# Optimization experiments

Hardware: AMD Instinct MI355X
Metric: run time of the kernel (lower is better)

Reference implementation:

```python
import jax, jax.numpy as jnp
import numpy as np

B, NQ, QDIM = 4, 128, 512
EMB, HEADS = 512, 8
VOCAB, WDIM = 20000, 300
DH = EMB // HEADS
TAU = 1.0
LN_EPS = 1e-5


def setup_inputs() -> dict:
    key = jax.random.key(0)
    ks = jax.random.split(key, 8)
    s = lambda fan_in: 1.0 / np.sqrt(fan_in)
    return {
        "queries": jax.random.normal(ks[0], (B, NQ, QDIM), dtype=jnp.float32),
        "glove": jax.random.normal(ks[1], (VOCAB, WDIM), dtype=jnp.float32),
        # Linear weights stored as (in, out); y = x @ W (equivalent to torch x @ W.T)
        "Wq": jax.random.normal(ks[2], (QDIM, EMB), dtype=jnp.float32) * s(QDIM),
        "Wk": jax.random.normal(ks[3], (WDIM, EMB), dtype=jnp.float32) * s(WDIM),
        "Wv": jax.random.normal(ks[4], (WDIM, EMB), dtype=jnp.float32) * s(WDIM),
        "Wout": jax.random.normal(ks[5], (EMB, QDIM), dtype=jnp.float32) * s(EMB),
        "b_out": jnp.zeros((QDIM,), dtype=jnp.float32),
        "ln_g": jnp.ones((QDIM,), dtype=jnp.float32),
        "ln_b": jnp.zeros((QDIM,), dtype=jnp.float32),
    }


def _forward(queries, glove, Wq, Wk, Wv, Wout, b_out, ln_g, ln_b):
    b, nq, _ = queries.shape
    V = glove.shape[0]
    scale = DH ** -0.5

    # SubLayerConnection: x + sublayer(LayerNorm(x))
    mu = jnp.mean(queries, axis=-1, keepdims=True)
    var = jnp.mean(jnp.square(queries - mu), axis=-1, keepdims=True)
    xn = (queries - mu) * jax.lax.rsqrt(var + LN_EPS) * ln_g + ln_b

    # Projections. K/V of the GloVe table are batch-independent -> compute once.
    q = (xn @ Wq).reshape(b, nq, HEADS, DH)          # [b, nq, h, dh]
    k = (glove @ Wk).reshape(V, HEADS, DH)           # [V, h, dh]
    v = (glove @ Wv).reshape(V, HEADS, DH)           # [V, h, dh]

    # Attention scores over the whole vocabulary: [b, h, nq, V]
    dots = jnp.einsum("bqhd,vhd->bhqv", q, k) * scale

    # Gumbel-softmax, hard (straight-through)
    gkey = jax.random.key(42)
    u = jax.random.uniform(gkey, dots.shape, dtype=dots.dtype,
                           minval=jnp.finfo(dots.dtype).tiny, maxval=1.0)
    gumbels = (dots - jnp.log(-jnp.log(u))) / TAU
    y_soft = jax.nn.softmax(gumbels, axis=-1)
    idx = jnp.argmax(gumbels, axis=-1)               # argmax(softmax) == argmax(logits)
    y_hard = jax.nn.one_hot(idx, V, dtype=dots.dtype)
    attn = y_hard - jax.lax.stop_gradient(y_soft) + y_soft

    out = jnp.einsum("bhqv,vhd->bqhd", attn, v).reshape(b, nq, EMB)
    out = out @ Wout + b_out                          # dropout is identity in eval
    return queries + out


def reference(queries, glove, Wq, Wk, Wv, Wout, b_out, ln_g, ln_b):
    return _forward(queries, glove, Wq, Wk, Wv, Wout, b_out, ln_g, ln_b)
```

## Files before the change

kernel.cpp:

```cpp
#include <hip/hip_runtime.h>
#include <cstdint>
#include <cmath>

#define NB 4
#define NQn 128
#define QD 512
#define EMBD 512
#define NH 8
#define DHn 64
#define VOCAB 20000
#define WDn 300
#define VCHUNK 128
#define NCHUNK 157

typedef float f32x4 __attribute__((ext_vector_type(4)));
typedef float f32x2 __attribute__((ext_vector_type(2)));
typedef short bf16x8 __attribute__((ext_vector_type(8)));

__device__ __forceinline__ f32x2 lo2(f32x4 v) { return __builtin_shufflevector(v, v, 0, 1); }
__device__ __forceinline__ f32x2 hi2(f32x4 v) { return __builtin_shufflevector(v, v, 2, 3); }

__device__ __forceinline__ void pk_fma_blo(f32x2 &d, f32x2 a, f32x2 b) {
  asm("v_pk_fma_f32 %0, %1, %2, %0 op_sel:[0,0,0] op_sel_hi:[0,1,1]"
      : "+v"(d) : "v"(a), "v"(b));
}
__device__ __forceinline__ void pk_fma_bhi(f32x2 &d, f32x2 a, f32x2 b) {
  asm("v_pk_fma_f32 %0, %1, %2, %0 op_sel:[1,0,0] op_sel_hi:[1,1,1]"
      : "+v"(d) : "v"(a), "v"(b));
}

__device__ __forceinline__ uint32_t rotl(uint32_t x, int r) {
  return __builtin_amdgcn_alignbit(x, x, 32 - r);
}

__device__ __forceinline__ uint32_t cvt_pk_bf16(float a, float b) {
  uint32_t r;
  asm("v_cvt_pk_bf16_f32 %0, %1, %2" : "=v"(r) : "v"(a), "v"(b));
  return r;
}

__device__ __forceinline__ void split4(f32x4 v, uint2 &hi, uint2 &lo) {
  uint32_t h01 = cvt_pk_bf16(v.x, v.y);
  uint32_t h23 = cvt_pk_bf16(v.z, v.w);
  float rx = v.x - __uint_as_float(h01 << 16);
  float ry = v.y - __uint_as_float(h01 & 0xFFFF0000u);
  float rz = v.z - __uint_as_float(h23 << 16);
  float rw = v.w - __uint_as_float(h23 & 0xFFFF0000u);
  hi = make_uint2(h01, h23);
  lo = make_uint2(cvt_pk_bf16(rx, ry), cvt_pk_bf16(rz, rw));
}

#define TFK1 42u
#define TFK2 (0x1BD11BDAu ^ 42u)
__device__ __forceinline__ void tf8(uint32_t (&x0)[8], uint32_t (&x1)[8]) {
#define R8(r) \
  { _Pragma("unroll") for (int j = 0; j < 8; ++j) { x0[j] += x1[j]; x1[j] = rotl(x1[j], r); x1[j] ^= x0[j]; } }
#define K8(a, b) \
  { _Pragma("unroll") for (int j = 0; j < 8; ++j) { x0[j] += (a); x1[j] += (b); } }
  K8(0u, TFK1)
  R8(13) R8(15) R8(26) R8(6)  K8(TFK1, TFK2 + 1u)
  R8(17) R8(29) R8(16) R8(24) K8(TFK2, 0u + 2u)
  R8(13) R8(15) R8(26) R8(6)  K8(0u, TFK1 + 3u)
  R8(17) R8(29) R8(16) R8(24) K8(TFK1, TFK2 + 4u)
  R8(13) R8(15) R8(26) R8(6)  K8(TFK2, 0u + 5u)
#undef R8
#undef K8
}

__device__ __forceinline__ float gumbel_from_bits(uint32_t bits) {
  float f = __uint_as_float((bits >> 9) | 0x3f800000u) - 1.0f;
  float u = fmaxf(f, 1.17549435e-38f);
  float t = __log2f(u);
  float s = __log2f(-t);
  return fmaf(0.69314718f, s, -0.36651292f);
}

__device__ __forceinline__ unsigned long long pack_key(float val, int idx) {
  uint32_t fb = __float_as_uint(val);
  uint32_t key = (fb & 0x80000000u) ? ~fb : (fb | 0x80000000u);
  return ((unsigned long long)key << 32) |
         (unsigned long long)(0xFFFFFFFFu - (uint32_t)idx);
}

__global__ __launch_bounds__(256, 4) void ln_qproj_kernel(
                                const float* __restrict__ queries,
                                const float* __restrict__ Wq,
                                const float* __restrict__ ln_g,
                                const float* __restrict__ ln_b,
                                ushort* __restrict__ qh_ws,
                                ushort* __restrict__ ql_ws) {
  __shared__ float xnT[QD][4];
  const int tid = threadIdx.x;
  const int wave = tid >> 6, lane = tid & 63;
  const int r0 = blockIdx.x * 4;
  const int r = r0 + wave;

  float vals[8];
  float s = 0.f;
#pragma unroll
  for (int j = 0; j < 8; ++j) { vals[j] = queries[r * QD + j * 64 + lane]; s += vals[j]; }
#pragma unroll
  for (int m = 32; m >= 1; m >>= 1) s += __shfl_xor(s, m, 64);
  const float mu = s * (1.f / 512.f);
  float ss = 0.f;
#pragma unroll
  for (int j = 0; j < 8; ++j) { float d = vals[j] - mu; ss += d * d; }
#pragma unroll
  for (int m = 32; m >= 1; m >>= 1) ss += __shfl_xor(ss, m, 64);
  const float rstd = 1.f / sqrtf(ss * (1.f / 512.f) + 1e-5f);
#pragma unroll
  for (int j = 0; j < 8; ++j) {
    int e = j * 64 + lane;
    xnT[e][wave] = (vals[j] - mu) * rstd * ln_g[e] + ln_b[e];
  }
  __syncthreads();

  const int e = blockIdx.y * 256 + tid;
  float a0 = 0.f, a1 = 0.f, a2 = 0.f, a3 = 0.f;
#pragma unroll 4
  for (int i = 0; i < QD; ++i) {
    f32x4 xv = *(const f32x4*)&xnT[i][0];
    float w = Wq[i * EMBD + e];
    a0 += xv.x * w; a1 += xv.y * w; a2 += xv.z * w; a3 += xv.w * w;
  }
  const int h = e >> 6, d = e & 63;
  float aa[4] = {a0, a1, a2, a3};
#pragma unroll
  for (int i = 0; i < 4; ++i) {
    float q = aa[i] * 0.125f;
    uint32_t hp = cvt_pk_bf16(q, q);
    float resid = q - __uint_as_float(hp << 16);
    uint32_t lp = cvt_pk_bf16(resid, resid);
    size_t off = ((size_t)h * 512 + (r0 + i)) * 64 + d;
    qh_ws[off] = (ushort)(hp & 0xFFFFu);
    ql_ws[off] = (ushort)(lp & 0xFFFFu);
  }
}

#define BKk 60
__global__ __launch_bounds__(256, 4) void kproj_kernel(
                             const float* __restrict__ glove,
                             const float* __restrict__ Wk,
                             ushort* __restrict__ kh_ws,
                             ushort* __restrict__ kl_ws) {
  const int id = blockIdx.x;
  const int lo = id & 7, h = (id >> 3) & 7, vg = (id >> 6) * 8 + lo;
  if (vg >= 313) return;
  const int v0 = vg * 64;
  const int n0 = h * 64;
  __shared__ float AsT[BKk][68];
  __shared__ float Bs[BKk][64];
  const int tid = threadIdx.x;
  const int ty = tid >> 4, tx = tid & 15;
  f32x2 acc2[4][2] = {};
  for (int s = 0; s < 5; ++s) {
    const int w0 = s * BKk;
    __syncthreads();
    for (int f = tid; f < 64 * 15; f += 256) {
      int row = f / 15, c4 = f % 15;
      int v = v0 + row;
      float4 g4 = (v < VOCAB) ? *(const float4*)&glove[(size_t)v * WDn + w0 + c4 * 4]
                              : make_float4(0.f, 0.f, 0.f, 0.f);
      AsT[c4 * 4 + 0][row] = g4.x;
      AsT[c4 * 4 + 1][row] = g4.y;
      AsT[c4 * 4 + 2][row] = g4.z;
      AsT[c4 * 4 + 3][row] = g4.w;
    }
    for (int f = tid; f < BKk * 16; f += 256) {
      int row = f / 16, c4 = f % 16;
      *(float4*)&Bs[row][c4 * 4] = *(const float4*)&Wk[(size_t)(w0 + row) * EMBD + n0 + c4 * 4];
    }
    __syncthreads();
#pragma unroll 4
    for (int w = 0; w < BKk; ++w) {
      f32x4 aq = *(const f32x4*)&AsT[w][ty * 4];
      f32x4 bv = *(const f32x4*)&Bs[w][tx * 4];
      f32x2 bl = lo2(bv), bh = hi2(bv);
      f32x2 a01 = lo2(aq), a23 = hi2(aq);
      pk_fma_blo(acc2[0][0], a01, bl); pk_fma_blo(acc2[0][1], a01, bh);
      pk_fma_bhi(acc2[1][0], a01, bl); pk_fma_bhi(acc2[1][1], a01, bh);
      pk_fma_blo(acc2[2][0], a23, bl); pk_fma_blo(acc2[2][1], a23, bh);
      pk_fma_bhi(acc2[3][0], a23, bl); pk_fma_bhi(acc2[3][1], a23, bh);
    }
  }
#pragma unroll
  for (int i = 0; i < 4; ++i) {
    int v = v0 + ty * 4 + i;
    if (v < VOCAB) {
      f32x4 kv = {acc2[i][0].x, acc2[i][0].y, acc2[i][1].x, acc2[i][1].y};
      uint2 hi, lo2v;
      split4(kv, hi, lo2v);
      size_t off = ((size_t)h * VOCAB + v) * 64 + tx * 4;
      *(uint2*)&kh_ws[off] = hi;
      *(uint2*)&kl_ws[off] = lo2v;
    }
  }
}

template<bool FULL>
__device__ __forceinline__ void score_epi(const f32x4 (&acc)[8],
                                          int v0, int tx, int ty, int rowtile, int h,
                                          unsigned long long* __restrict__ pk_buf) {
#pragma unroll
  for (int i = 0; i < 4; ++i) {
    const int r = rowtile * 128 + ty * 4 + i;
    const int b = r >> 7, q = r & 127;
    const int rowidx = (b * NH + h) * NQn + q;
    const uint32_t base = (uint32_t)rowidx * (uint32_t)VOCAB;

    uint32_t x0[8], x1[8];
#pragma unroll
    for (int j = 0; j < 8; ++j) {
      x0[j] = 0u;
      x1[j] = base + (uint32_t)(v0 + tx + 16 * j);
    }
    tf8(x0, x1);

    float best = -INFINITY; int bidx = 0x7fffffff;
#pragma unroll
    for (int j = 0; j < 8; ++j) {
      int v = v0 + tx + 16 * j;
      if (FULL || v < VOCAB) {
        float g = gumbel_from_bits(x0[j] ^ x1[j]);
        float val = acc[j][i] - g;
        if (val > best) { best = val; bidx = v; }
      }
    }
#pragma unroll
    for (int m = 8; m >= 1; m >>= 1) {
      float ov = __shfl_xor(best, m, 64);
      int   oi = __shfl_xor(bidx, m, 64);
      if (ov > best || (ov == best && oi < bidx)) { best = ov; bidx = oi; }
    }
    if (tx == 0) atomicMax(&pk_buf[rowidx], pack_key(best, bidx));
  }
}

__global__ __launch_bounds__(512, 8) void score_kernel(
                  const ushort* __restrict__ qh_ws,
                  const ushort* __restrict__ ql_ws,
                  const ushort* __restrict__ kh_ws,
                  const ushort* __restrict__ kl_ws,
                  unsigned long long* __restrict__ pk_buf) {
  __shared__ uint4 lds4[2048];
  char* const Kh = (char*)lds4;
  char* const Kl = Kh + 16384;
  const int tid = threadIdx.x;
  const int id = blockIdx.x;
  const int h = id & 7, rowtile = (id >> 3) & 3, chunk = id >> 5;
  const int v0 = chunk * VCHUNK;
  const int tx = tid & 15, ty = tid >> 4;
  const int w = tid >> 6;
  const int g4 = (tid >> 4) & 3;
  const int swz = (tx & 7) << 4;

  bf16x8 aH[2], aL[2];
  {
    const size_t qbase = ((size_t)h * 512 + rowtile * 128 + w * 16 + tx) * 64 + g4 * 8;
#pragma unroll
    for (int kh = 0; kh < 2; ++kh) {
      aH[kh] = *(const bf16x8*)(qh_ws + qbase + kh * 32);
      aL[kh] = *(const bf16x8*)(ql_ws + qbase + kh * 32);
    }
  }

  for (int f = tid; f < 128 * 8; f += 512) {
    int row = f >> 3, c8 = f & 7;
    int v = v0 + row;
    uint4 vh = {0u, 0u, 0u, 0u}, vl = {0u, 0u, 0u, 0u};
    if (v < VOCAB) {
      size_t off = ((size_t)h * VOCAB + v) * 64 + c8 * 8;
      vh = *(const uint4*)(kh_ws + off);
      vl = *(const uint4*)(kl_ws + off);
    }
    int loff = (row * 128 + c8 * 16) ^ ((row & 7) << 4);
    *(uint4*)(Kh + loff) = vh;
    *(uint4*)(Kl + loff) = vl;
  }
  __syncthreads();

  f32x4 acc[8] = {};
#pragma unroll
  for (int ct = 0; ct < 8; ++ct) {
    const int bbase = (ct * 16 + tx) * 128 + g4 * 16;
    bf16x8 bH[2], bL[2];
#pragma unroll
    for (int kh = 0; kh < 2; ++kh) {
      int off = (bbase + kh * 64) ^ swz;
      bH[kh] = *(const bf16x8*)(Kh + off);
      bL[kh] = *(const bf16x8*)(Kl + off);
    }
    acc[ct] = __builtin_amdgcn_mfma_f32_16x16x32_bf16(aH[0], bH[0], acc[ct], 0, 0, 0);
    acc[ct] = __builtin_amdgcn_mfma_f32_16x16x32_bf16(aH[1], bH[1], acc[ct], 0, 0, 0);
    acc[ct] = __builtin_amdgcn_mfma_f32_16x16x32_bf16(aH[0], bL[0], acc[ct], 0, 0, 0);
    acc[ct] = __builtin_amdgcn_mfma_f32_16x16x32_bf16(aH[1], bL[1], acc[ct], 0, 0, 0);
    acc[ct] = __builtin_amdgcn_mfma_f32_16x16x32_bf16(aL[0], bH[0], acc[ct], 0, 0, 0);
    acc[ct] = __builtin_amdgcn_mfma_f32_16x16x32_bf16(aL[1], bH[1], acc[ct], 0, 0, 0);
    acc[ct] = __builtin_amdgcn_mfma_f32_16x16x32_bf16(aL[0], bL[0], acc[ct], 0, 0, 0);
    acc[ct] = __builtin_amdgcn_mfma_f32_16x16x32_bf16(aL[1], bL[1], acc[ct], 0, 0, 0);
  }

  if (v0 + VCHUNK <= VOCAB)
    score_epi<true>(acc, v0, tx, ty, rowtile, h, pk_buf);
  else
    score_epi<false>(acc, v0, tx, ty, rowtile, h, pk_buf);
}

__global__ __launch_bounds__(512, 8) void out_kernel(
                           const float* __restrict__ queries,
                           const float* __restrict__ glove,
                           const float* __restrict__ Wv,
                           const float* __restrict__ Wout,
                           const float* __restrict__ b_out,
                           const unsigned long long* __restrict__ pk_buf,
                           float* __restrict__ out) {
  __shared__ float gl[NH][WDn];
  __shared__ float vrow[EMBD];
  __shared__ int idxs[NH];
  const int tid = threadIdx.x;
  const int r = blockIdx.x, b = r >> 7, q = r & 127;
  if (tid < NH) {
    unsigned long long p = pk_buf[(b * NH + tid) * NQn + q];
    idxs[tid] = (int)(0xFFFFFFFFu - (uint32_t)(p & 0xFFFFFFFFull));
  }
  __syncthreads();
  for (int f = tid; f < NH * 75; f += 512) {
    int hh = f / 75, c4 = f % 75;
    *(float4*)&gl[hh][c4 * 4] = *(const float4*)&glove[(size_t)idxs[hh] * WDn + c4 * 4];
  }
  __syncthreads();
  {
    const int e = tid, hh = e >> 6;
    float a = 0.f;
    for (int w = 0; w < WDn; ++w) a += gl[hh][w] * Wv[(size_t)w * EMBD + e];
    vrow[e] = a;
  }
  __syncthreads();
  {
    const int j = tid;
    float o = 0.f;
    for (int e = 0; e < EMBD; ++e) o += vrow[e] * Wout[(size_t)e * QD + j];
    out[(size_t)r * QD + j] = queries[(size_t)r * QD + j] + o + b_out[j];
  }
}

extern "C" void kernel_launch(void* const* d_in, const int* in_sizes, int n_in,
                              void* d_out, int out_size, void* d_ws, size_t ws_size,
                              hipStream_t stream) {
  const float* queries = (const float*)d_in[0];
  const float* glove   = (const float*)d_in[1];
  const float* Wq      = (const float*)d_in[2];
  const float* Wk      = (const float*)d_in[3];
  const float* Wv      = (const float*)d_in[4];
  const float* Wout    = (const float*)d_in[5];
  const float* b_out   = (const float*)d_in[6];
  const float* ln_g    = (const float*)d_in[7];
  const float* ln_b    = (const float*)d_in[8];
  float* out = (float*)d_out;

  char* ws = (char*)d_ws;
  ushort* qh_ws = (ushort*)ws;
  ushort* ql_ws = qh_ws + (size_t)NH * 512 * 64;
  ushort* kh_ws = ql_ws + (size_t)NH * 512 * 64;
  ushort* kl_ws = kh_ws + (size_t)NH * VOCAB * 64;
  unsigned long long* pk_buf = (unsigned long long*)(kl_ws + (size_t)NH * VOCAB * 64);

  hipMemsetAsync(pk_buf, 0, (size_t)NB * NH * NQn * sizeof(unsigned long long), stream);

  hipLaunchKernelGGL(ln_qproj_kernel, dim3(128, 2), dim3(256), 0, stream,
                     queries, Wq, ln_g, ln_b, qh_ws, ql_ws);
  hipLaunchKernelGGL(kproj_kernel, dim3(2560), dim3(256), 0, stream,
                     glove, Wk, kh_ws, kl_ws);
  hipLaunchKernelGGL(score_kernel, dim3(5024), dim3(512), 0, stream,
                     qh_ws, ql_ws, kh_ws, kl_ws, pk_buf);
  hipLaunchKernelGGL(out_kernel, dim3(512), dim3(512), 0, stream,
                     queries, glove, Wv, Wout, b_out, pk_buf, out);
}
```

Measured before the change: 346.7 us.

## Merge Q/K projection kernels and pk_buf memset into one prep launch

The LayerNorm+Q-projection kernel, the K-projection kernel and the memset of the argmax buffer become a single launch, with each role picked from the block index. This removes two launch gaps and the memset, and lets the small Q-projection blocks run alongside the K-projection blocks. The Gumbel subtraction is folded into one fma, and the Q fragment loads in the score kernel move after the K tile staging to overlap with it. The merged kernel uses a shared LDS buffer sized for the larger role, so the Q-projection blocks reserve more LDS than they need.

```diff
diff --git a/kernel.cpp b/kernel.cpp
--- a/kernel.cpp
+++ b/kernel.cpp
@@ -67,14 +67,6 @@
 #undef K8
 }
 
-__device__ __forceinline__ float gumbel_from_bits(uint32_t bits) {
-  float f = __uint_as_float((bits >> 9) | 0x3f800000u) - 1.0f;
-  float u = fmaxf(f, 1.17549435e-38f);
-  float t = __log2f(u);
-  float s = __log2f(-t);
-  return fmaf(0.69314718f, s, -0.36651292f);
-}
-
 __device__ __forceinline__ unsigned long long pack_key(float val, int idx) {
   uint32_t fb = __float_as_uint(val);
   uint32_t key = (fb & 0x80000000u) ? ~fb : (fb | 0x80000000u);
@@ -82,118 +74,124 @@
          (unsigned long long)(0xFFFFFFFFu - (uint32_t)idx);
 }
 
-__global__ __launch_bounds__(256, 4) void ln_qproj_kernel(
-                                const float* __restrict__ queries,
-                                const float* __restrict__ Wq,
-                                const float* __restrict__ ln_g,
-                                const float* __restrict__ ln_b,
-                                ushort* __restrict__ qh_ws,
-                                ushort* __restrict__ ql_ws) {
-  __shared__ float xnT[QD][4];
-  const int tid = threadIdx.x;
-  const int wave = tid >> 6, lane = tid & 63;
-  const int r0 = blockIdx.x * 4;
-  const int r = r0 + wave;
-
-  float vals[8];
-  float s = 0.f;
-#pragma unroll
-  for (int j = 0; j < 8; ++j) { vals[j] = queries[r * QD + j * 64 + lane]; s += vals[j]; }
-#pragma unroll
-  for (int m = 32; m >= 1; m >>= 1) s += __shfl_xor(s, m, 64);
-  const float mu = s * (1.f / 512.f);
-  float ss = 0.f;
-#pragma unroll
-  for (int j = 0; j < 8; ++j) { float d = vals[j] - mu; ss += d * d; }
-#pragma unroll
-  for (int m = 32; m >= 1; m >>= 1) ss += __shfl_xor(ss, m, 64);
-  const float rstd = 1.f / sqrtf(ss * (1.f / 512.f) + 1e-5f);
-#pragma unroll
-  for (int j = 0; j < 8; ++j) {
-    int e = j * 64 + lane;
-    xnT[e][wave] = (vals[j] - mu) * rstd * ln_g[e] + ln_b[e];
-  }
-  __syncthreads();
-
-  const int e = blockIdx.y * 256 + tid;
-  float a0 = 0.f, a1 = 0.f, a2 = 0.f, a3 = 0.f;
-#pragma unroll 4
-  for (int i = 0; i < QD; ++i) {
-    f32x4 xv = *(const f32x4*)&xnT[i][0];
-    float w = Wq[i * EMBD + e];
-    a0 += xv.x * w; a1 += xv.y * w; a2 += xv.z * w; a3 += xv.w * w;
-  }
-  const int h = e >> 6, d = e & 63;
-  float aa[4] = {a0, a1, a2, a3};
-#pragma unroll
-  for (int i = 0; i < 4; ++i) {
-    float q = aa[i] * 0.125f;
-    uint32_t hp = cvt_pk_bf16(q, q);
-    float resid = q - __uint_as_float(hp << 16);
-    uint32_t lp = cvt_pk_bf16(resid, resid);
-    size_t off = ((size_t)h * 512 + (r0 + i)) * 64 + d;
-    qh_ws[off] = (ushort)(hp & 0xFFFFu);
-    ql_ws[off] = (ushort)(lp & 0xFFFFu);
-  }
-}
-
 #define BKk 60
-__global__ __launch_bounds__(256, 4) void kproj_kernel(
+__global__ __launch_bounds__(256, 4) void prep_kernel(
+                             const float* __restrict__ queries,
+                             const float* __restrict__ Wq,
+                             const float* __restrict__ ln_g,
+                             const float* __restrict__ ln_b,
                              const float* __restrict__ glove,
                              const float* __restrict__ Wk,
+                             ushort* __restrict__ qh_ws,
+                             ushort* __restrict__ ql_ws,
                              ushort* __restrict__ kh_ws,
-                             ushort* __restrict__ kl_ws) {
-  const int id = blockIdx.x;
-  const int lo = id & 7, h = (id >> 3) & 7, vg = (id >> 6) * 8 + lo;
-  if (vg >= 313) return;
-  const int v0 = vg * 64;
-  const int n0 = h * 64;
-  __shared__ float AsT[BKk][68];
-  __shared__ float Bs[BKk][64];
+                             ushort* __restrict__ kl_ws,
+                             unsigned long long* __restrict__ pk_buf) {
+  __shared__ __align__(16) char smem[31680];
+  const int bid = blockIdx.x;
   const int tid = threadIdx.x;
-  const int ty = tid >> 4, tx = tid & 15;
-  f32x2 acc2[4][2] = {};
-  for (int s = 0; s < 5; ++s) {
-    const int w0 = s * BKk;
+
+  if (bid < 2560) {
+    const int lo = bid & 7, h = (bid >> 3) & 7, vg = (bid >> 6) * 8 + lo;
+    if (vg >= 313) return;
+    const int v0 = vg * 64;
+    const int n0 = h * 64;
+    float (*AsT)[68] = (float(*)[68])smem;
+    float (*Bs)[64]  = (float(*)[64])(smem + 16320);
+    const int ty = tid >> 4, tx = tid & 15;
+    f32x2 acc2[4][2] = {};
+    for (int s = 0; s < 5; ++s) {
+      const int w0 = s * BKk;
+      __syncthreads();
+      for (int f = tid; f < 64 * 15; f += 256) {
+        int row = f / 15, c4 = f % 15;
+        int v = v0 + row;
+        float4 g4 = (v < VOCAB) ? *(const float4*)&glove[(size_t)v * WDn + w0 + c4 * 4]
+                                : make_float4(0.f, 0.f, 0.f, 0.f);
+        AsT[c4 * 4 + 0][row] = g4.x;
+        AsT[c4 * 4 + 1][row] = g4.y;
+        AsT[c4 * 4 + 2][row] = g4.z;
+        AsT[c4 * 4 + 3][row] = g4.w;
+      }
+      for (int f = tid; f < BKk * 16; f += 256) {
+        int row = f / 16, c4 = f % 16;
+        *(float4*)&Bs[row][c4 * 4] = *(const float4*)&Wk[(size_t)(w0 + row) * EMBD + n0 + c4 * 4];
+      }
+      __syncthreads();
+#pragma unroll 4
+      for (int w = 0; w < BKk; ++w) {
+        f32x4 aq = *(const f32x4*)&AsT[w][ty * 4];
+        f32x4 bv = *(const f32x4*)&Bs[w][tx * 4];
+        f32x2 bl = lo2(bv), bh = hi2(bv);
+        f32x2 a01 = lo2(aq), a23 = hi2(aq);
+        pk_fma_blo(acc2[0][0], a01, bl); pk_fma_blo(acc2[0][1], a01, bh);
+        pk_fma_bhi(acc2[1][0], a01, bl); pk_fma_bhi(acc2[1][1], a01, bh);
+        pk_fma_blo(acc2[2][0], a23, bl); pk_fma_blo(acc2[2][1], a23, bh);
+        pk_fma_bhi(acc2[3][0], a23, bl); pk_fma_bhi(acc2[3][1], a23, bh);
+      }
+    }
+#pragma unroll
+    for (int i = 0; i < 4; ++i) {
+      int v = v0 + ty * 4 + i;
+      if (v < VOCAB) {
+        f32x4 kv = {acc2[i][0].x, acc2[i][0].y, acc2[i][1].x, acc2[i][1].y};
+        uint2 hi, lov;
+        split4(kv, hi, lov);
+        size_t off = ((size_t)h * VOCAB + v) * 64 + tx * 4;
+        *(uint2*)&kh_ws[off] = hi;
+        *(uint2*)&kl_ws[off] = lov;
+      }
+    }
+  } else if (bid < 2816) {
+    const int id = bid - 2560;
+    const int bx = id & 127, by = id >> 7;
+    float (*xnT)[4] = (float(*)[4])smem;
+    const int wave = tid >> 6, lane = tid & 63;
+    const int r0 = bx * 4;
+    const int r = r0 + wave;
+
+    float vals[8];
+    float s = 0.f;
+#pragma unroll
+    for (int j = 0; j < 8; ++j) { vals[j] = queries[r * QD + j * 64 + lane]; s += vals[j]; }
+#pragma unroll
+    for (int m = 32; m >= 1; m >>= 1) s += __shfl_xor(s, m, 64);
+    const float mu = s * (1.f / 512.f);
+    float ss = 0.f;
+#pragma unroll
+    for (int j = 0; j < 8; ++j) { float d = vals[j] - mu; ss += d * d; }
+#pragma unroll
+    for (int m = 32; m >= 1; m >>= 1) ss += __shfl_xor(ss, m, 64);
+    const float rstd = 1.f / sqrtf(ss * (1.f / 512.f) + 1e-5f);
+#pragma unroll
+    for (int j = 0; j < 8; ++j) {
+      int e = j * 64 + lane;
+      xnT[e][wave] = (vals[j] - mu) * rstd * ln_g[e] + ln_b[e];
+    }
     __syncthreads();
-    for (int f = tid; f < 64 * 15; f += 256) {
-      int row = f / 15, c4 = f % 15;
-      int v = v0 + row;
-      float4 g4 = (v < VOCAB) ? *(const float4*)&glove[(size_t)v * WDn + w0 + c4 * 4]
-                              : make_float4(0.f, 0.f, 0.f, 0.f);
-      AsT[c4 * 4 + 0][row] = g4.x;
-      AsT[c4 * 4 + 1][row] = g4.y;
-      AsT[c4 * 4 + 2][row] = g4.z;
-      AsT[c4 * 4 + 3][row] = g4.w;
-    }
-    for (int f = tid; f < BKk * 16; f += 256) {
-      int row = f / 16, c4 = f % 16;
-      *(float4*)&Bs[row][c4 * 4] = *(const float4*)&Wk[(size_t)(w0 + row) * EMBD + n0 + c4 * 4];
-    }
-    __syncthreads();
+
+    const int e = by * 256 + tid;
+    float a0 = 0.f, a1 = 0.f, a2 = 0.f, a3 = 0.f;
 #pragma unroll 4
-    for (int w = 0; w < BKk; ++w) {
-      f32x4 aq = *(const f32x4*)&AsT[w][ty * 4];
-      f32x4 bv = *(const f32x4*)&Bs[w][tx * 4];
-      f32x2 bl = lo2(bv), bh = hi2(bv);
-      f32x2 a01 = lo2(aq), a23 = hi2(aq);
-      pk_fma_blo(acc2[0][0], a01, bl); pk_fma_blo(acc2[0][1], a01, bh);
-      pk_fma_bhi(acc2[1][0], a01, bl); pk_fma_bhi(acc2[1][1], a01, bh);
-      pk_fma_blo(acc2[2][0], a23, bl); pk_fma_blo(acc2[2][1], a23, bh);
-      pk_fma_bhi(acc2[3][0], a23, bl); pk_fma_bhi(acc2[3][1], a23, bh);
-    }
-  }
-#pragma unroll
-  for (int i = 0; i < 4; ++i) {
-    int v = v0 + ty * 4 + i;
-    if (v < VOCAB) {
-      f32x4 kv = {acc2[i][0].x, acc2[i][0].y, acc2[i][1].x, acc2[i][1].y};
-      uint2 hi, lo2v;
-      split4(kv, hi, lo2v);
-      size_t off = ((size_t)h * VOCAB + v) * 64 + tx * 4;
-      *(uint2*)&kh_ws[off] = hi;
-      *(uint2*)&kl_ws[off] = lo2v;
-    }
+    for (int i = 0; i < QD; ++i) {
+      f32x4 xv = *(const f32x4*)&xnT[i][0];
+      float w = Wq[i * EMBD + e];
+      a0 += xv.x * w; a1 += xv.y * w; a2 += xv.z * w; a3 += xv.w * w;
+    }
+    const int h = e >> 6, d = e & 63;
+    float aa[4] = {a0, a1, a2, a3};
+#pragma unroll
+    for (int i = 0; i < 4; ++i) {
+      float q = aa[i] * 0.125f;
+      uint32_t hp = cvt_pk_bf16(q, q);
+      float resid = q - __uint_as_float(hp << 16);
+      uint32_t lp = cvt_pk_bf16(resid, resid);
+      size_t off = ((size_t)h * 512 + (r0 + i)) * 64 + d;
+      qh_ws[off] = (ushort)(hp & 0xFFFFu);
+      ql_ws[off] = (ushort)(lp & 0xFFFFu);
+    }
+  } else {
+    for (int f = tid; f < NB * NH * NQn; f += 256) pk_buf[f] = 0ull;
   }
 }
 
@@ -221,8 +219,12 @@
     for (int j = 0; j < 8; ++j) {
       int v = v0 + tx + 16 * j;
       if (FULL || v < VOCAB) {
-        float g = gumbel_from_bits(x0[j] ^ x1[j]);
-        float val = acc[j][i] - g;
+        uint32_t bits = x0[j] ^ x1[j];
+        float f = __uint_as_float((bits >> 9) | 0x3f800000u) - 1.0f;
+        float u = fmaxf(f, 1.17549435e-38f);
+        float t = __log2f(u);
+        float s = __log2f(-t);
+        float val = fmaf(-0.69314718f, s, acc[j][i]);
         if (val > best) { best = val; bidx = v; }
       }
     }
@@ -254,16 +256,6 @@
   const int g4 = (tid >> 4) & 3;
   const int swz = (tx & 7) << 4;
 
-  bf16x8 aH[2], aL[2];
-  {
-    const size_t qbase = ((size_t)h * 512 + rowtile * 128 + w * 16 + tx) * 64 + g4 * 8;
-#pragma unroll
-    for (int kh = 0; kh < 2; ++kh) {
-      aH[kh] = *(const bf16x8*)(qh_ws + qbase + kh * 32);
-      aL[kh] = *(const bf16x8*)(ql_ws + qbase + kh * 32);
-    }
-  }
-
   for (int f = tid; f < 128 * 8; f += 512) {
     int row = f >> 3, c8 = f & 7;
     int v = v0 + row;
@@ -276,6 +268,16 @@
     int loff = (row * 128 + c8 * 16) ^ ((row & 7) << 4);
     *(uint4*)(Kh + loff) = vh;
     *(uint4*)(Kl + loff) = vl;
+  }
+
+  bf16x8 aH[2], aL[2];
+  {
+    const size_t qbase = ((size_t)h * 512 + rowtile * 128 + w * 16 + tx) * 64 + g4 * 8;
+#pragma unroll
+    for (int kh = 0; kh < 2; ++kh) {
+      aH[kh] = *(const bf16x8*)(qh_ws + qbase + kh * 32);
+      aL[kh] = *(const bf16x8*)(ql_ws + qbase + kh * 32);
+    }
   }
   __syncthreads();
 
@@ -365,12 +367,9 @@
   ushort* kl_ws = kh_ws + (size_t)NH * VOCAB * 64;
   unsigned long long* pk_buf = (unsigned long long*)(kl_ws + (size_t)NH * VOCAB * 64);
 
-  hipMemsetAsync(pk_buf, 0, (size_t)NB * NH * NQn * sizeof(unsigned long long), stream);
-
-  hipLaunchKernelGGL(ln_qproj_kernel, dim3(128, 2), dim3(256), 0, stream,
-                     queries, Wq, ln_g, ln_b, qh_ws, ql_ws);
-  hipLaunchKernelGGL(kproj_kernel, dim3(2560), dim3(256), 0, stream,
-                     glove, Wk, kh_ws, kl_ws);
+  hipLaunchKernelGGL(prep_kernel, dim3(2817), dim3(256), 0, stream,
+                     queries, Wq, ln_g, ln_b, glove, Wk,
+                     qh_ws, ql_ws, kh_ws, kl_ws, pk_buf);
   hipLaunchKernelGGL(score_kernel, dim3(5024), dim3(512), 0, stream,
                      qh_ws, ql_ws, kh_ws, kl_ws, pk_buf);
   hipLaunchKernelGGL(out_kernel, dim3(512), dim3(512), 0, stream,
```

After: 316.8 us. 1.09x faster.
